# Kernel tuning notes

Measured on AMD Instinct MI355X. Metric: run time of the kernel, lower is better.

The kernel has to match this reference:

```python
import jax, jax.numpy as jnp
import numpy as np


def _conv(x, w, b=None, stride=1, pad=0, dil=1):
    out = jax.lax.conv_general_dilated(
        x, w, (stride, stride), [(pad, pad), (pad, pad)],
        rhs_dilation=(dil, dil),
        dimension_numbers=('NCHW', 'OIHW', 'NCHW'))
    return out if b is None else out + b[None, :, None, None]


def _sobel_base(out_ch, in_ch, k=3):
    # Exactly mirrors SobelConv2d weight construction (4 directional kernels).
    w = np.zeros((out_ch, in_ch, k, k), np.float32)
    m = k // 2
    for idx in range(out_ch):
        if idx % 4 == 0:
            w[idx, :, 0, :] = -1; w[idx, :, 0, m] = -2
            w[idx, :, -1, :] = 1; w[idx, :, -1, m] = 2
        elif idx % 4 == 1:
            w[idx, :, :, 0] = -1; w[idx, :, m, 0] = -2
            w[idx, :, :, -1] = 1; w[idx, :, m, -1] = 2
        elif idx % 4 == 2:
            w[idx, :, 0, 0] = -2
            for i in range(m + 1):
                w[idx, :, m - i, i] = -1
                w[idx, :, k - 1 - i, m + i] = 1
            w[idx, :, -1, -1] = 2
        else:
            w[idx, :, -1, 0] = -2
            for i in range(m + 1):
                w[idx, :, m + i, i] = -1
                w[idx, :, i, m + i] = 1
            w[idx, :, 0, -1] = 2
    return w


def setup_inputs() -> dict:
    key = jax.random.key(0)
    ks = iter(jax.random.split(key, 40))
    def p(shape, s=0.05):
        return jax.random.normal(next(ks), shape, dtype=jnp.float32) * s
    C = 32  # out_ch == sobel_ch
    f32 = jnp.float32
    return dict(
        x=jax.random.normal(next(ks), (8, 1, 256, 256), dtype=f32),
        sobel_base=jnp.asarray(_sobel_base(C, 1)),
        sobel_factor=jnp.ones((C, 1, 1, 1), f32),
        sobel_bias=jnp.zeros((C,), f32),
        f4_w=p((C, C + 1, 3, 3)), f4_b=jnp.zeros((C,), f32),
        ec1_w=p((C, C, 3, 3)), ec1_b=jnp.zeros((C,), f32),
        ec2_w=p((C, C, 3, 3)), ec2_b=jnp.zeros((C,), f32),
        ec3_w=p((C, C, 3, 3)), ec3_b=jnp.zeros((C,), f32),
        gate_w=p((3, 3 * C, 1, 1)), gate_b=jnp.zeros((3,), f32),
        ca1_w=p((C // 16, C, 1, 1)),  # ChannelAttention fc1 (ratio=16), no bias
        ca2_w=p((C, C // 16, 1, 1)),  # fc2, no bias
        sa_w=p((1, 2, 7, 7)),         # SpatialAttention conv, no bias
        p1_w=p((C, C, 1, 1)), p1_b=jnp.zeros((C,), f32),
        f1_w=p((C, C, 3, 3)), f1_b=jnp.zeros((C,), f32),
        p2_w=p((C, 2 * C, 1, 1)), p2_b=jnp.zeros((C,), f32),
        f2_w=p((C, C, 3, 3)), f2_b=jnp.zeros((C,), f32),
        p3_w=p((C, 2 * C, 1, 1)), p3_b=jnp.zeros((C,), f32),
        f3_w=p((C, C, 3, 3)), f3_b=jnp.zeros((C,), f32),
    )


def reference(x, sobel_base, sobel_factor, sobel_bias, f4_w, f4_b,
              ec1_w, ec1_b, ec2_w, ec2_b, ec3_w, ec3_b, gate_w, gate_b,
              ca1_w, ca2_w, sa_w,
              p1_w, p1_b, f1_w, f1_b, p2_w, p2_b, f2_w, f2_b,
              p3_w, p3_b, f3_w, f3_b):
    lrelu = lambda t: jax.nn.leaky_relu(t, 0.01)
    relu = jax.nn.relu
    # Sobel edge extraction (fixed directional kernels scaled by learned factor)
    out0 = _conv(x, sobel_base * sobel_factor, sobel_bias, pad=1)     # [B,32,H,W]
    out1 = jnp.concatenate([x, out0], axis=1)                          # [B,33,H,W]
    out1 = lrelu(_conv(out1, f4_w, f4_b, pad=1))                       # [B,32,H,W]
    # AdaptiveEdgeConnector: multi-dilation convs + softmax gating
    ex = relu(_conv(out1, ec1_w, ec1_b, pad=1))
    ey = relu(_conv(out1, ec2_w, ec2_b, pad=2, dil=2))
    ez = relu(_conv(out1, ec3_w, ec3_b, pad=3, dil=3))
    gates = jax.nn.softmax(_conv(jnp.concatenate([ex, ey, ez], axis=1), gate_w, gate_b), axis=1)
    enh = gates[:, 0:1] * ex + gates[:, 1:2] * ey + gates[:, 2:3] * ez
    # CBAM: channel attention
    avg = jnp.mean(enh, axis=(2, 3), keepdims=True)
    mx = jnp.max(enh, axis=(2, 3), keepdims=True)
    ca = jax.nn.sigmoid(_conv(relu(_conv(avg, ca1_w)), ca2_w)
                        + _conv(relu(_conv(mx, ca1_w)), ca2_w))
    f = ca * enh
    # CBAM: spatial attention
    sa_in = jnp.concatenate([jnp.mean(f, axis=1, keepdims=True),
                             jnp.max(f, axis=1, keepdims=True)], axis=1)
    sa = jax.nn.sigmoid(_conv(sa_in, sa_w, pad=3))
    edge = sa * f
    # Residual merge + cascaded dense conv stages
    out0 = lrelu(out1 + edge)
    t = lrelu(_conv(out0, p1_w, p1_b))
    t = lrelu(_conv(t, f1_w, f1_b, pad=1))
    o1 = jnp.concatenate([out0, t], axis=1)                            # [B,64,H,W]
    t = lrelu(_conv(o1, p2_w, p2_b))
    t = lrelu(_conv(t, f2_w, f2_b, pad=1))
    o2 = jnp.concatenate([out0, t], axis=1)
    t = lrelu(_conv(o2, p3_w, p3_b))
    t = lrelu(_conv(t, f3_w, f3_b, pad=1))
    return jnp.concatenate([out0, t], axis=1)                          # [B,64,H,W]
```

## Files before the change

kernel.cpp:

```cpp
#include <hip/hip_runtime.h>
#include <math.h>

typedef unsigned short u16;
typedef short short8 __attribute__((ext_vector_type(8)));
typedef float f32x4 __attribute__((ext_vector_type(4)));
typedef unsigned short ushort4v __attribute__((ext_vector_type(4)));

#define Hh 256
#define Ww 256
#define Bb 8
#define PW 262
#define PAD 3
#define HPW (Hh * PW)

__device__ __forceinline__ float bf2f(u16 v) {
    unsigned u = ((unsigned)v) << 16;
    union { unsigned u; float f; } c; c.u = u; return c.f;
}
__device__ __forceinline__ u16 f2bf(float f) {
    union { float f; unsigned u; } c; c.f = f;
    unsigned lsb = (c.u >> 16) & 1u;
    c.u += 0x7fffu + lsb;
    return (u16)(c.u >> 16);
}
__device__ __forceinline__ float sigm(float v) { return 1.f / (1.f + expf(-v)); }

template<int ACT, bool F32OUT>
__global__ __launch_bounds__(256) void convs_k(
    const u16* __restrict__ in, const u16* __restrict__ apack,
    const float* __restrict__ bias, void* __restrict__ outp)
{
    __shared__ u16 rows[3][4352];
    const int tid = threadIdx.x, lane = tid & 63, wv = tid >> 6;
    const int b = blockIdx.x & 7;
    const int rest = blockIdx.x >> 3;
    const int h = rest >> 1, half = rest & 1;
    const int pl = wv * 32 + (lane & 15);
    const int icg = lane >> 4;

    for (int idx = tid; idx < 3 * 536; idx += 256) {
        int rr = idx / 536, q = idx % 536;
        int r = h - 1 + rr;
        short8 v = (short8){0, 0, 0, 0, 0, 0, 0, 0};
        if ((unsigned)r < 256u)
            v = *(const short8*)(in + ((size_t)b * HPW + (size_t)r * PW + PAD + half * 128 - 3) * 32
                                 + (size_t)q * 8);
        *(short8*)(&rows[rr][q * 8]) = v;
    }
    __syncthreads();

    f32x4 acc[2][2];
    #pragma unroll
    for (int mf = 0; mf < 2; ++mf)
        #pragma unroll
        for (int nf = 0; nf < 2; ++nf)
            acc[mf][nf] = (f32x4){0.f, 0.f, 0.f, 0.f};

    #pragma unroll
    for (int tap = 0; tap < 9; ++tap) {
        const int kh = tap / 3 - 1, kw = tap % 3 - 1;
        const int ri = 1 + kh;
        short8 a0 = *(const short8*)(apack + ((size_t)(tap * 2 + 0) * 64 + lane) * 8);
        short8 a1 = *(const short8*)(apack + ((size_t)(tap * 2 + 1) * 64 + lane) * 8);
        #pragma unroll
        for (int nf = 0; nf < 2; ++nf) {
            short8 bf = *(const short8*)(&rows[ri][(pl + nf * 16 + kw + 3) * 32 + icg * 8]);
            acc[0][nf] = __builtin_amdgcn_mfma_f32_16x16x32_bf16(a0, bf, acc[0][nf], 0, 0, 0);
            acc[1][nf] = __builtin_amdgcn_mfma_f32_16x16x32_bf16(a1, bf, acc[1][nf], 0, 0, 0);
        }
    }
    const int nl = half * 128 + pl;
    f32x4 bi[2];
    bi[0] = *(const f32x4*)(bias + icg * 4);
    bi[1] = *(const f32x4*)(bias + 16 + icg * 4);
    if (F32OUT) {
        float* dp = (float*)outp + ((size_t)b * 64 + 32) * 65536 + (size_t)h * 256;
        #pragma unroll
        for (int mf = 0; mf < 2; ++mf) {
            const int cob = mf * 16 + icg * 4;
            #pragma unroll
            for (int nf = 0; nf < 2; ++nf) {
                const int w = nl + nf * 16;
                #pragma unroll
                for (int i = 0; i < 4; ++i) {
                    float v = acc[mf][nf][i] + bi[mf][i];
                    if (ACT == 1) v = fmaxf(v, 0.f);
                    if (ACT == 2) v = (v > 0.f) ? v : 0.01f * v;
                    dp[(size_t)(cob + i) * 65536 + w] = v;
                }
            }
        }
    } else {
        const size_t orow = ((size_t)b * HPW + (size_t)h * PW + PAD) * 32;
        u16* out = (u16*)outp;
        #pragma unroll
        for (int mf = 0; mf < 2; ++mf) {
            const int cob = mf * 16 + icg * 4;
            #pragma unroll
            for (int nf = 0; nf < 2; ++nf) {
                ushort4v o;
                #pragma unroll
                for (int i = 0; i < 4; ++i) {
                    float v = acc[mf][nf][i] + bi[mf][i];
                    if (ACT == 1) v = fmaxf(v, 0.f);
                    if (ACT == 2) v = (v > 0.f) ? v : 0.01f * v;
                    o[i] = f2bf(v);
                }
                *(ushort4v*)(out + orow + (size_t)(nl + nf * 16) * 32 + cob) = o;
            }
        }
    }
}

__global__ __launch_bounds__(256) void ecfuse_k(
    const u16* __restrict__ in, const u16* __restrict__ apack,
    const float* __restrict__ b1, const float* __restrict__ b2,
    const float* __restrict__ b3, const float* __restrict__ gw_,
    const float* __restrict__ gb_, u16* __restrict__ enh)
{
    __shared__ u16 rows[3][4352];
    __shared__ float gw[288];
    __shared__ float gb[3];
    __shared__ float bs[96];
    int tid = threadIdx.x;
    for (int i = tid; i < 288; i += 256) gw[i] = gw_[i];
    if (tid < 3) gb[tid] = gb_[tid];
    if (tid < 32) bs[tid] = b1[tid];
    else if (tid < 64) bs[tid] = b2[tid - 32];
    else if (tid < 96) bs[tid] = b3[tid - 64];

    const int lane = tid & 63, wv = tid >> 6;
    const int b = blockIdx.x & 7;
    const int rest = blockIdx.x >> 3;
    const int h = rest >> 1, half = rest & 1;
    const int pl = wv * 32 + (lane & 15);
    const int icg = lane >> 4;

    f32x4 acc[3][2][2];
    #pragma unroll
    for (int cv = 0; cv < 3; ++cv)
        #pragma unroll
        for (int mf = 0; mf < 2; ++mf)
            #pragma unroll
            for (int nf = 0; nf < 2; ++nf)
                acc[cv][mf][nf] = (f32x4){0.f, 0.f, 0.f, 0.f};

    #pragma unroll
    for (int cv = 0; cv < 3; ++cv) {
        const int dil = cv + 1;
        __syncthreads();
        for (int idx = tid; idx < 3 * 536; idx += 256) {
            int rr = idx / 536, q = idx % 536;
            int r = h + (rr - 1) * dil;
            short8 v = (short8){0, 0, 0, 0, 0, 0, 0, 0};
            if ((unsigned)r < 256u)
                v = *(const short8*)(in + ((size_t)b * HPW + (size_t)r * PW + PAD + half * 128 - 3) * 32
                                     + (size_t)q * 8);
            *(short8*)(&rows[rr][q * 8]) = v;
        }
        __syncthreads();
        #pragma unroll
        for (int tap = 0; tap < 9; ++tap) {
            const int kh = tap / 3 - 1, kw = tap % 3 - 1;
            const int ri = 1 + kh;
            const int s = cv * 9 + tap;
            short8 a0 = *(const short8*)(apack + ((size_t)(s * 2 + 0) * 64 + lane) * 8);
            short8 a1 = *(const short8*)(apack + ((size_t)(s * 2 + 1) * 64 + lane) * 8);
            #pragma unroll
            for (int nf = 0; nf < 2; ++nf) {
                short8 bf = *(const short8*)(&rows[ri][(pl + nf * 16 + kw * dil + 3) * 32 + icg * 8]);
                acc[cv][0][nf] = __builtin_amdgcn_mfma_f32_16x16x32_bf16(a0, bf, acc[cv][0][nf], 0, 0, 0);
                acc[cv][1][nf] = __builtin_amdgcn_mfma_f32_16x16x32_bf16(a1, bf, acc[cv][1][nf], 0, 0, 0);
            }
        }
    }
    const int nl = half * 128 + pl;
    const size_t orow = ((size_t)b * HPW + (size_t)h * PW + PAD) * 32;
    #pragma unroll
    for (int nf = 0; nf < 2; ++nf) {
        float e[3][2][4];
        float g0 = 0.f, g1 = 0.f, g2 = 0.f;
        #pragma unroll
        for (int cv = 0; cv < 3; ++cv)
            #pragma unroll
            for (int mf = 0; mf < 2; ++mf) {
                const int cob = mf * 16 + icg * 4;
                #pragma unroll
                for (int i = 0; i < 4; ++i) {
                    float v = fmaxf(acc[cv][mf][nf][i] + bs[cv * 32 + cob + i], 0.f);
                    e[cv][mf][i] = v;
                    const int c = cv * 32 + cob + i;
                    g0 = fmaf(gw[c], v, g0);
                    g1 = fmaf(gw[96 + c], v, g1);
                    g2 = fmaf(gw[192 + c], v, g2);
                }
            }
        g0 += __shfl_xor(g0, 16); g0 += __shfl_xor(g0, 32);
        g1 += __shfl_xor(g1, 16); g1 += __shfl_xor(g1, 32);
        g2 += __shfl_xor(g2, 16); g2 += __shfl_xor(g2, 32);
        g0 += gb[0]; g1 += gb[1]; g2 += gb[2];
        float m = fmaxf(g0, fmaxf(g1, g2));
        float e0 = expf(g0 - m), e1 = expf(g1 - m), e2 = expf(g2 - m);
        float inv = 1.f / (e0 + e1 + e2);
        e0 *= inv; e1 *= inv; e2 *= inv;
        #pragma unroll
        for (int mf = 0; mf < 2; ++mf) {
            const int cob = mf * 16 + icg * 4;
            ushort4v o;
            #pragma unroll
            for (int i = 0; i < 4; ++i)
                o[i] = f2bf(e0 * e[0][mf][i] + e1 * e[1][mf][i] + e2 * e[2][mf][i]);
            *(ushort4v*)(enh + orow + (size_t)(nl + nf * 16) * 32 + cob) = o;
        }
    }
}

template<int ICB, int ACT, bool TWO>
__global__ __launch_bounds__(256) void convm_k(
    const u16* __restrict__ in0, const u16* __restrict__ in1,
    const u16* __restrict__ apack, const float* __restrict__ bias,
    u16* __restrict__ out)
{
    constexpr int CS = TWO ? 32 : ICB * 32;
    const int tid = threadIdx.x, lane = tid & 63, wv = tid >> 6;
    const int b = blockIdx.x & 7, h = blockIdx.x >> 3;
    const int nl = (wv << 6) + (lane & 15);
    const int icg = lane >> 4;

    f32x4 acc[2][4];
    #pragma unroll
    for (int mf = 0; mf < 2; ++mf)
        #pragma unroll
        for (int nf = 0; nf < 4; ++nf)
            acc[mf][nf] = (f32x4){0.f, 0.f, 0.f, 0.f};

    #pragma unroll
    for (int s = 0; s < ICB; ++s) {
        short8 a0 = *(const short8*)(apack + ((size_t)(s * 2 + 0) * 64 + lane) * 8);
        short8 a1 = *(const short8*)(apack + ((size_t)(s * 2 + 1) * 64 + lane) * 8);
        const u16* src = TWO ? (s ? in1 : in0) : in0;
        const int icoff = TWO ? 0 : s * 32;
        size_t base = ((size_t)b * HPW + (size_t)h * PW + PAD + nl) * CS + icoff + icg * 8;
        #pragma unroll
        for (int nf = 0; nf < 4; ++nf) {
            short8 bf = *(const short8*)(src + base + (size_t)nf * 16 * CS);
            acc[0][nf] = __builtin_amdgcn_mfma_f32_16x16x32_bf16(a0, bf, acc[0][nf], 0, 0, 0);
            acc[1][nf] = __builtin_amdgcn_mfma_f32_16x16x32_bf16(a1, bf, acc[1][nf], 0, 0, 0);
        }
    }
    const size_t orow = ((size_t)b * HPW + (size_t)h * PW + PAD) * 32;
    #pragma unroll
    for (int mf = 0; mf < 2; ++mf) {
        const int cob = mf * 16 + icg * 4;
        f32x4 bi = *(const f32x4*)(bias + cob);
        #pragma unroll
        for (int nf = 0; nf < 4; ++nf) {
            ushort4v o;
            #pragma unroll
            for (int i = 0; i < 4; ++i) {
                float v = acc[mf][nf][i] + bi[i];
                if (ACT == 1) v = fmaxf(v, 0.f);
                if (ACT == 2) v = (v > 0.f) ? v : 0.01f * v;
                o[i] = f2bf(v);
            }
            *(ushort4v*)(out + orow + (size_t)(nl + nf * 16) * 32 + cob) = o;
        }
    }
}

__global__ void prepack_k(
    const float* __restrict__ f4w, const float* __restrict__ e1w,
    const float* __restrict__ e2w, const float* __restrict__ e3w,
    const float* __restrict__ f1w, const float* __restrict__ f2w,
    const float* __restrict__ f3w, const float* __restrict__ p1w,
    const float* __restrict__ p2w, const float* __restrict__ p3w,
    u16* __restrict__ apack)
{
    int gid = blockIdx.x * 256 + threadIdx.x;
    if (gid >= 77 * 1024) return;
    const int offs[11] = {0, 18, 27, 36, 45, 54, 63, 72, 73, 75, 77};
    int step = gid >> 10, r = gid & 1023;
    int layer = 0;
    while (step >= offs[layer + 1]) layer++;
    int s = step - offs[layer];
    int mf = r >> 9, l = (r >> 3) & 63, j = r & 7;
    int co = mf * 16 + (l & 15);
    int ICB = (layer == 0 || layer == 8 || layer == 9) ? 2 : 1;
    int tap = s / ICB, icb = s % ICB;
    int icl = icb * 32 + (l >> 4) * 8 + j;
    float v = 0.f;
    if (layer == 0)      { if (icl < 33) v = f4w[(co * 33 + icl) * 9 + tap]; }
    else if (layer == 1) v = e1w[(co * 32 + icl) * 9 + tap];
    else if (layer == 2) v = e2w[(co * 32 + icl) * 9 + tap];
    else if (layer == 3) v = e3w[(co * 32 + icl) * 9 + tap];
    else if (layer == 4) v = f1w[(co * 32 + icl) * 9 + tap];
    else if (layer == 5) v = f2w[(co * 32 + icl) * 9 + tap];
    else if (layer == 6) v = f3w[(co * 32 + icl) * 9 + tap];
    else if (layer == 7) v = p1w[co * 32 + icl];
    else if (layer == 8) v = p2w[co * 64 + icl];
    else                 v = p3w[co * 64 + icl];
    apack[gid] = f2bf(v);
}

__global__ void bzero_k(u16* __restrict__ buf, int total)
{
    int idx = blockIdx.x * 256 + threadIdx.x;
    if (idx >= total) return;
    int c = idx & 31, r = idx >> 5;
    int col6 = r % 6, h = (r / 6) & 255, b = r / (6 * 256);
    int col = (col6 < 3) ? col6 : (256 + PAD + col6 - 3);
    buf[((size_t)b * HPW + (size_t)h * PW + col) * 32 + c] = 0;
}

__global__ __launch_bounds__(256) void prep5_k(
    const float* __restrict__ f4w, const float* __restrict__ f4b,
    const float* __restrict__ sbase, const float* __restrict__ sfac,
    const float* __restrict__ sbias,
    float* __restrict__ w5, float* __restrict__ be)
{
    __shared__ float sF[32 * 33 * 9];
    __shared__ float sS[288];
    __shared__ float sBias[32];
    int t = threadIdx.x;
    for (int i = t; i < 32 * 33 * 9; i += 256) sF[i] = f4w[i];
    for (int i = t; i < 288; i += 256) sS[i] = sbase[i] * sfac[i / 9];
    if (t < 32) sBias[t] = sbias[t];
    __syncthreads();

    for (int idx = t; idx < 800; idx += 256) {
        int co = idx / 25, tap = idx % 25, kh = tap / 5, kw = tap % 5;
        float s = 0.f;
        if (kh >= 1 && kh <= 3 && kw >= 1 && kw <= 3)
            s = sF[(co * 33 + 0) * 9 + (kh - 1) * 3 + (kw - 1)];
        for (int sc = 0; sc < 32; ++sc) {
            #pragma unroll
            for (int a = 0; a < 3; ++a)
                #pragma unroll
                for (int bq = 0; bq < 3; ++bq) {
                    int p = kh - a, q = kw - bq;
                    if (p >= 0 && p < 3 && q >= 0 && q < 3)
                        s = fmaf(sF[(co * 33 + 1 + sc) * 9 + a * 3 + bq],
                                 sS[sc * 9 + p * 3 + q], s);
                }
        }
        w5[idx] = s;
    }
    for (int co = t; co < 32; co += 256) {
        float s = f4b[co];
        for (int sc = 0; sc < 32; ++sc) {
            float wsum = 0.f;
            #pragma unroll
            for (int k = 0; k < 9; ++k) wsum += sF[(co * 33 + 1 + sc) * 9 + k];
            s = fmaf(sBias[sc], wsum, s);
        }
        be[co] = s;
    }
}

__global__ __launch_bounds__(256) void conv5_k(
    const float* __restrict__ x, const float* __restrict__ w5,
    const float* __restrict__ be, u16* __restrict__ out1)
{
    __shared__ float sw[800];
    __shared__ float sb[32];
    int tid = threadIdx.x;
    for (int i = tid; i < 800; i += 256) sw[i] = w5[i];
    if (tid < 32) sb[tid] = be[tid];
    __syncthreads();
    int b = blockIdx.x & 7, h = blockIdx.x >> 3, w = tid;
    const float* xp = x + (size_t)b * 65536;
    float xv[25];
    #pragma unroll
    for (int i = 0; i < 5; ++i) {
        int r = h + i - 2;
        #pragma unroll
        for (int j = 0; j < 5; ++j) {
            int c = w + j - 2;
            xv[i * 5 + j] = ((unsigned)r < 256u && (unsigned)c < 256u)
                            ? xp[r * 256 + c] : 0.f;
        }
    }
    u16* dst = out1 + ((size_t)b * HPW + (size_t)h * PW + PAD + w) * 32;
    #pragma unroll
    for (int cb = 0; cb < 4; ++cb) {
        short8 o;
        #pragma unroll
        for (int j = 0; j < 8; ++j) {
            int co = cb * 8 + j;
            float s = sb[co];
            #pragma unroll
            for (int t2 = 0; t2 < 25; ++t2) s = fmaf(sw[co * 25 + t2], xv[t2], s);
            s = (s > 0.f) ? s : 0.01f * s;
            o[j] = (short)f2bf(s);
        }
        *(short8*)(dst + cb * 8) = o;
    }
}

__global__ __launch_bounds__(256) void ringfix_k(
    const float* __restrict__ x, const float* __restrict__ f4w,
    const float* __restrict__ f4b, const float* __restrict__ sbase,
    const float* __restrict__ sfac, const float* __restrict__ sbias,
    u16* __restrict__ out1)
{
    __shared__ float sW[288];
    __shared__ float sB[32];
    __shared__ float sF[32 * 33 * 9];
    __shared__ float sO[66][2][32];
    int tid = threadIdx.x;
    for (int i = tid; i < 288; i += 256) sW[i] = sbase[i] * sfac[i / 9];
    if (tid < 32) sB[tid] = sbias[tid];
    for (int i = tid; i < 32 * 33 * 9; i += 256) sF[i] = f4w[i];
    __syncthreads();

    int blk = blockIdx.x;
    int b = blk & 7, rest = blk >> 3;
    int e = rest >> 2, seg = rest & 3;
    const float* xp = x + (size_t)b * 65536;

    for (int i = tid; i < 66 * 2 * 32; i += 256) {
        int sc = i & 31, rr2 = i >> 5;
        int d = rr2 & 1, ul = rr2 >> 1;
        int ug = seg * 64 - 1 + ul;
        float v = 0.f;
        if ((unsigned)ug < 256u) {
            int h, w;
            if (e == 0)      { h = d;        w = ug; }
            else if (e == 1) { h = 255 - d;  w = ug; }
            else if (e == 2) { h = ug;       w = d; }
            else             { h = ug;       w = 255 - d; }
            float s = sB[sc];
            for (int p = 0; p < 3; ++p)
                for (int q = 0; q < 3; ++q) {
                    int rr = h + p - 1, cc = w + q - 1;
                    if ((unsigned)rr < 256u && (unsigned)cc < 256u)
                        s = fmaf(sW[sc * 9 + p * 3 + q], xp[rr * 256 + cc], s);
                }
            v = s;
        }
        sO[ul][d][sc] = v;
    }
    __syncthreads();

    int pi = tid & 63, cog = tid >> 6;
    int up = seg * 64 + pi;
    int h, w;
    if (e == 0)      { h = 0;   w = up; }
    else if (e == 1) { h = 255; w = up; }
    else if (e == 2) { h = up;  w = 0; }
    else             { h = up;  w = 255; }
    short8 ov;
    for (int cj = 0; cj < 8; ++cj) {
        int co = cog * 8 + cj;
        float acc = f4b[co];
        for (int a = 0; a < 3; ++a)
            for (int bb = 0; bb < 3; ++bb) {
                int hh = h + a - 1, ww = w + bb - 1;
                if ((unsigned)hh < 256u && (unsigned)ww < 256u)
                    acc = fmaf(sF[(co * 33) * 9 + a * 3 + bb], xp[hh * 256 + ww], acc);
                int d, ug;
                if (e == 0)      { d = hh;        ug = ww; }
                else if (e == 1) { d = 255 - hh;  ug = ww; }
                else if (e == 2) { d = ww;        ug = hh; }
                else             { d = 255 - ww;  ug = hh; }
                if (d >= 0 && d < 2 && (unsigned)ug < 256u) {
                    int ul = ug - (seg * 64 - 1);
                    for (int sc = 0; sc < 32; ++sc)
                        acc = fmaf(sF[(co * 33 + 1 + sc) * 9 + a * 3 + bb], sO[ul][d][sc], acc);
                }
            }
        acc = (acc > 0.f) ? acc : 0.01f * acc;
        ov[cj] = (short)f2bf(acc);
    }
    u16* dst = out1 + ((size_t)b * HPW + (size_t)h * PW + PAD + w) * 32 + cog * 8;
    *(short8*)dst = ov;
}

__global__ __launch_bounds__(256) void ca_part_k(
    const u16* __restrict__ enh, float* __restrict__ part)
{
    int blk = blockIdx.x, b = blk & 7, sl = blk >> 3;
    int tid = threadIdx.x, lane = tid & 63, wv = tid >> 6;
    float s[32], m[32];
    #pragma unroll
    for (int c = 0; c < 32; ++c) { s[c] = 0.f; m[c] = -1e30f; }
    for (int k = 0; k < 8; ++k) {
        int px = sl * 2048 + k * 256 + tid;
        int h = px >> 8, w = px & 255;
        size_t off = ((size_t)b * HPW + (size_t)h * PW + PAD + w) * 32;
        #pragma unroll
        for (int cb = 0; cb < 4; ++cb) {
            short8 v = *(const short8*)(enh + off + cb * 8);
            #pragma unroll
            for (int j = 0; j < 8; ++j) {
                float f = bf2f((u16)v[j]);
                s[cb * 8 + j] += f;
                m[cb * 8 + j] = fmaxf(m[cb * 8 + j], f);
            }
        }
    }
    #pragma unroll
    for (int c = 0; c < 32; ++c)
        #pragma unroll
        for (int o = 32; o; o >>= 1) {
            s[c] += __shfl_down(s[c], o);
            m[c] = fmaxf(m[c], __shfl_down(m[c], o));
        }
    __shared__ float ls[4][32], lm[4][32];
    if (lane == 0)
        for (int c = 0; c < 32; ++c) { ls[wv][c] = s[c]; lm[wv][c] = m[c]; }
    __syncthreads();
    if (tid < 32) {
        float ts = 0.f, tm = -1e30f;
        for (int w2 = 0; w2 < 4; ++w2) { ts += ls[w2][tid]; tm = fmaxf(tm, lm[w2][tid]); }
        int bs = b * 32 + sl;
        part[(size_t)(bs * 2 + 0) * 32 + tid] = ts;
        part[(size_t)(bs * 2 + 1) * 32 + tid] = tm;
    }
}

__global__ void ca_final_k(const float* __restrict__ part,
                           const float* __restrict__ w1, const float* __restrict__ w2,
                           float* __restrict__ ca)
{
    int t = threadIdx.x, b = t >> 5, c = t & 31;
    float s = 0.f, m = -1e30f;
    for (int sl = 0; sl < 32; ++sl) {
        int bs = b * 32 + sl;
        s += part[(size_t)(bs * 2 + 0) * 32 + c];
        m = fmaxf(m, part[(size_t)(bs * 2 + 1) * 32 + c]);
    }
    __shared__ float av[8][32], mx[8][32];
    av[b][c] = s * (1.f / 65536.f);
    mx[b][c] = m;
    __syncthreads();
    float sa0 = 0.f, sm0 = 0.f, sa1 = 0.f, sm1 = 0.f;
    for (int k = 0; k < 32; ++k) {
        float wa = w1[k], wb = w1[32 + k];
        sa0 = fmaf(wa, av[b][k], sa0); sm0 = fmaf(wa, mx[b][k], sm0);
        sa1 = fmaf(wb, av[b][k], sa1); sm1 = fmaf(wb, mx[b][k], sm1);
    }
    float h0 = fmaxf(sa0, 0.f) + fmaxf(sm0, 0.f);
    float h1 = fmaxf(sa1, 0.f) + fmaxf(sm1, 0.f);
    ca[t] = sigm(w2[c * 2 + 0] * h0 + w2[c * 2 + 1] * h1);
}

__global__ __launch_bounds__(256) void samap_k(
    const u16* __restrict__ enh, const float* __restrict__ ca,
    float* __restrict__ smap)
{
    __shared__ float sca[256];
    int tid = threadIdx.x;
    sca[tid] = ca[tid];
    __syncthreads();
    int b = blockIdx.x & 7;
    int r = (blockIdx.x >> 3) * 256 + tid;
    if (r >= 262 * 262) return;
    int ph = r / 262, pw = r % 262;
    float mean = 0.f, mxv = 0.f;
    if (ph >= 3 && ph < 259 && pw >= 3 && pw < 259) {
        int h = ph - 3, w = pw - 3;
        size_t off = ((size_t)b * HPW + (size_t)h * PW + PAD + w) * 32;
        float s = 0.f, m = -1e30f;
        #pragma unroll
        for (int cb = 0; cb < 4; ++cb) {
            short8 v = *(const short8*)(enh + off + cb * 8);
            #pragma unroll
            for (int j = 0; j < 8; ++j) {
                float f = bf2f((u16)v[j]) * sca[b * 32 + cb * 8 + j];
                s += f; m = fmaxf(m, f);
            }
        }
        mean = s * (1.f / 32.f); mxv = m;
    }
    smap[((size_t)b * 262 * 262 + (size_t)ph * 262 + pw) * 2 + 0] = mean;
    smap[((size_t)b * 262 * 262 + (size_t)ph * 262 + pw) * 2 + 1] = mxv;
}

__global__ __launch_bounds__(256) void merge_k(
    const float* __restrict__ smap, const float* __restrict__ saw,
    const float* __restrict__ ca, const u16* __restrict__ out1,
    const u16* __restrict__ enh, u16* __restrict__ o0,
    float* __restrict__ dout)
{
    __shared__ float sw[98];
    __shared__ float sca[256];
    int tid = threadIdx.x;
    for (int i = tid; i < 98; i += 256) sw[i] = saw[i];
    sca[tid] = ca[tid];
    __syncthreads();
    int b = blockIdx.x & 7;
    int hw = (blockIdx.x >> 3) * 256 + tid;
    int h = hw >> 8, w = hw & 255;
    const float* sp = smap + (size_t)b * 262 * 262 * 2;
    float acc = 0.f;
    #pragma unroll
    for (int kh = 0; kh < 7; ++kh)
        #pragma unroll
        for (int kw = 0; kw < 7; ++kw) {
            const float* q = sp + ((size_t)(h + kh) * 262 + (w + kw)) * 2;
            acc = fmaf(q[0], sw[kh * 7 + kw], acc);
            acc = fmaf(q[1], sw[49 + kh * 7 + kw], acc);
        }
    float sa = sigm(acc);
    size_t off = ((size_t)b * HPW + (size_t)h * PW + PAD + w) * 32;
    float* dp = dout + (size_t)b * 64 * 65536 + hw;
    #pragma unroll
    for (int cb = 0; cb < 4; ++cb) {
        short8 ve = *(const short8*)(enh + off + cb * 8);
        short8 vo = *(const short8*)(out1 + off + cb * 8);
        short8 o;
        #pragma unroll
        for (int j = 0; j < 8; ++j) {
            float f = sca[b * 32 + cb * 8 + j] * bf2f((u16)ve[j]);
            float v = bf2f((u16)vo[j]) + sa * f;
            v = (v > 0.f) ? v : 0.01f * v;
            o[j] = (short)f2bf(v);
            dp[(size_t)(cb * 8 + j) * 65536] = v;
        }
        *(short8*)(o0 + off + cb * 8) = o;
    }
}

extern "C" void kernel_launch(void* const* d_in, const int* in_sizes, int n_in,
                              void* d_out, int out_size, void* d_ws, size_t ws_size,
                              hipStream_t stream)
{
    (void)in_sizes; (void)n_in; (void)out_size; (void)ws_size;
    const float* x        = (const float*)d_in[0];
    const float* sob_base = (const float*)d_in[1];
    const float* sob_fac  = (const float*)d_in[2];
    const float* sob_bias = (const float*)d_in[3];
    const float* f4_w = (const float*)d_in[4];   const float* f4_b = (const float*)d_in[5];
    const float* ec1_w = (const float*)d_in[6];  const float* ec1_b = (const float*)d_in[7];
    const float* ec2_w = (const float*)d_in[8];  const float* ec2_b = (const float*)d_in[9];
    const float* ec3_w = (const float*)d_in[10]; const float* ec3_b = (const float*)d_in[11];
    const float* gate_w = (const float*)d_in[12]; const float* gate_b = (const float*)d_in[13];
    const float* ca1_w = (const float*)d_in[14]; const float* ca2_w = (const float*)d_in[15];
    const float* sa_w  = (const float*)d_in[16];
    const float* p1_w = (const float*)d_in[17]; const float* p1_b = (const float*)d_in[18];
    const float* f1_w = (const float*)d_in[19]; const float* f1_b = (const float*)d_in[20];
    const float* p2_w = (const float*)d_in[21]; const float* p2_b = (const float*)d_in[22];
    const float* f2_w = (const float*)d_in[23]; const float* f2_b = (const float*)d_in[24];
    const float* p3_w = (const float*)d_in[25]; const float* p3_b = (const float*)d_in[26];
    const float* f3_w = (const float*)d_in[27]; const float* f3_b = (const float*)d_in[28];

    const size_t PB32 = (size_t)Bb * HPW * 32 * 2;
    char* ws = (char*)d_ws;
    u16* Q    = (u16*)(ws);
    u16* O0   = (u16*)(ws + PB32);
    u16* T    = (u16*)(ws + 2 * PB32);
    u16* ENH  = (u16*)(ws + 3 * PB32);
    u16* AP   = (u16*)(ws + 4 * PB32);
    float* W5   = (float*)(ws + 4 * PB32 + 77 * 1024 * 2);
    float* BE   = W5 + 800;
    float* PART = BE + 32;
    float* CA   = PART + 8 * 32 * 2 * 32;

    char* doutc = (char*)d_out;
    float* SMAP = (float*)(doutc + (134217728 - (size_t)Bb * 262 * 262 * 2 * 4));
    float* dout = (float*)d_out;

    dim3 blk(256);

    prepack_k<<<308, blk, 0, stream>>>(f4_w, ec1_w, ec2_w, ec3_w, f1_w, f2_w, f3_w,
                                       p1_w, p2_w, p3_w, AP);
    prep5_k<<<1, blk, 0, stream>>>(f4_w, f4_b, sob_base, sob_fac, sob_bias, W5, BE);
    bzero_k<<<1536, blk, 0, stream>>>(Q, Bb * 256 * 6 * 32);
    bzero_k<<<1536, blk, 0, stream>>>(T, Bb * 256 * 6 * 32);
    conv5_k<<<2048, blk, 0, stream>>>(x, W5, BE, Q);
    ringfix_k<<<128, blk, 0, stream>>>(x, f4_w, f4_b, sob_base, sob_fac, sob_bias, Q);
    ecfuse_k<<<4096, blk, 0, stream>>>(Q, AP + 18 * 1024, ec1_b, ec2_b, ec3_b,
                                       gate_w, gate_b, ENH);
    ca_part_k<<<256, blk, 0, stream>>>(ENH, PART);
    ca_final_k<<<1, blk, 0, stream>>>(PART, ca1_w, ca2_w, CA);
    samap_k<<<2152, blk, 0, stream>>>(ENH, CA, SMAP);
    merge_k<<<2048, blk, 0, stream>>>(SMAP, sa_w, CA, Q, ENH, O0, dout);
    convm_k<1, 2, false><<<2048, blk, 0, stream>>>(O0, nullptr, AP + 72 * 1024, p1_b, Q);
    convs_k<2, false><<<4096, blk, 0, stream>>>(Q, AP + 45 * 1024, f1_b, T);
    convm_k<2, 2, true ><<<2048, blk, 0, stream>>>(O0, T, AP + 73 * 1024, p2_b, Q);
    convs_k<2, false><<<4096, blk, 0, stream>>>(Q, AP + 54 * 1024, f2_b, T);
    convm_k<2, 2, true ><<<2048, blk, 0, stream>>>(O0, T, AP + 75 * 1024, p3_b, Q);
    convs_k<2, true ><<<4096, blk, 0, stream>>>(Q, AP + 63 * 1024, f3_b, dout);
}
```

Before: 437.8 us.

## Swizzle LDS row layout, prefetch weight fragments, stage f32 outputs through LDS

Reorganises the shared-memory row buffers in the 3x3 conv kernels into channel-group-major order to reduce bank conflicts on MFMA operand reads, and prefetches the next tap's weight fragments into registers. The fp32 output stores in the final conv and merge kernels are staged through LDS and written as 16-byte vectors. One zero-fill launch for the T buffer is dropped, which relies on its halo columns staying zero otherwise. The extra LDS tile in merge may reduce occupancy.

```diff
diff --git a/kernel.cpp b/kernel.cpp
--- a/kernel.cpp
+++ b/kernel.cpp
@@ -24,6 +24,7 @@
     return (u16)(c.u >> 16);
 }
 __device__ __forceinline__ float sigm(float v) { return 1.f / (1.f + expf(-v)); }
+
 
 template<int ACT, bool F32OUT>
 __global__ __launch_bounds__(256) void convs_k(
@@ -40,12 +41,13 @@
 
     for (int idx = tid; idx < 3 * 536; idx += 256) {
         int rr = idx / 536, q = idx % 536;
+        int p = q >> 2, g = q & 3;
         int r = h - 1 + rr;
         short8 v = (short8){0, 0, 0, 0, 0, 0, 0, 0};
         if ((unsigned)r < 256u)
             v = *(const short8*)(in + ((size_t)b * HPW + (size_t)r * PW + PAD + half * 128 - 3) * 32
-                                 + (size_t)q * 8);
-        *(short8*)(&rows[rr][q * 8]) = v;
+                                 + (size_t)p * 32 + g * 8);
+        *(short8*)(&rows[rr][(g * 136 + p) * 8]) = v;
     }
     __syncthreads();
 
@@ -56,40 +58,54 @@
         for (int nf = 0; nf < 2; ++nf)
             acc[mf][nf] = (f32x4){0.f, 0.f, 0.f, 0.f};
 
+    short8 a0c = *(const short8*)(apack + (size_t)(0 * 2 + 0) * 512 + lane * 8);
+    short8 a1c = *(const short8*)(apack + (size_t)(0 * 2 + 1) * 512 + lane * 8);
     #pragma unroll
     for (int tap = 0; tap < 9; ++tap) {
         const int kh = tap / 3 - 1, kw = tap % 3 - 1;
         const int ri = 1 + kh;
-        short8 a0 = *(const short8*)(apack + ((size_t)(tap * 2 + 0) * 64 + lane) * 8);
-        short8 a1 = *(const short8*)(apack + ((size_t)(tap * 2 + 1) * 64 + lane) * 8);
+        short8 a0n, a1n;
+        if (tap < 8) {
+            a0n = *(const short8*)(apack + (size_t)((tap + 1) * 2 + 0) * 512 + lane * 8);
+            a1n = *(const short8*)(apack + (size_t)((tap + 1) * 2 + 1) * 512 + lane * 8);
+        }
         #pragma unroll
         for (int nf = 0; nf < 2; ++nf) {
-            short8 bf = *(const short8*)(&rows[ri][(pl + nf * 16 + kw + 3) * 32 + icg * 8]);
-            acc[0][nf] = __builtin_amdgcn_mfma_f32_16x16x32_bf16(a0, bf, acc[0][nf], 0, 0, 0);
-            acc[1][nf] = __builtin_amdgcn_mfma_f32_16x16x32_bf16(a1, bf, acc[1][nf], 0, 0, 0);
-        }
+            short8 bf = *(const short8*)(&rows[ri][(icg * 136 + pl + nf * 16 + kw + 3) * 8]);
+            acc[0][nf] = __builtin_amdgcn_mfma_f32_16x16x32_bf16(a0c, bf, acc[0][nf], 0, 0, 0);
+            acc[1][nf] = __builtin_amdgcn_mfma_f32_16x16x32_bf16(a1c, bf, acc[1][nf], 0, 0, 0);
+        }
+        a0c = a0n; a1c = a1n;
     }
     const int nl = half * 128 + pl;
     f32x4 bi[2];
     bi[0] = *(const f32x4*)(bias + icg * 4);
     bi[1] = *(const f32x4*)(bias + 16 + icg * 4);
     if (F32OUT) {
-        float* dp = (float*)outp + ((size_t)b * 64 + 32) * 65536 + (size_t)h * 256;
+        float* ldsf = (float*)&rows[0][0];
+        __syncthreads();
         #pragma unroll
         for (int mf = 0; mf < 2; ++mf) {
             const int cob = mf * 16 + icg * 4;
             #pragma unroll
             for (int nf = 0; nf < 2; ++nf) {
-                const int w = nl + nf * 16;
+                const int pxl = pl + nf * 16;
                 #pragma unroll
                 for (int i = 0; i < 4; ++i) {
                     float v = acc[mf][nf][i] + bi[mf][i];
                     if (ACT == 1) v = fmaxf(v, 0.f);
                     if (ACT == 2) v = (v > 0.f) ? v : 0.01f * v;
-                    dp[(size_t)(cob + i) * 65536 + w] = v;
+                    ldsf[(cob + i) * 128 + pxl] = v;
                 }
             }
         }
+        __syncthreads();
+        const int ch = tid >> 3, pxb = (tid & 7) * 16;
+        float* dp = (float*)outp + ((size_t)b * 64 + 32 + ch) * 65536
+                    + (size_t)h * 256 + half * 128 + pxb;
+        #pragma unroll
+        for (int j = 0; j < 4; ++j)
+            *(f32x4*)(dp + j * 4) = *(f32x4*)(&ldsf[ch * 128 + pxb + j * 4]);
     } else {
         const size_t orow = ((size_t)b * HPW + (size_t)h * PW + PAD) * 32;
         u16* out = (u16*)outp;
@@ -151,27 +167,34 @@
         __syncthreads();
         for (int idx = tid; idx < 3 * 536; idx += 256) {
             int rr = idx / 536, q = idx % 536;
+            int p = q >> 2, g = q & 3;
             int r = h + (rr - 1) * dil;
             short8 v = (short8){0, 0, 0, 0, 0, 0, 0, 0};
             if ((unsigned)r < 256u)
                 v = *(const short8*)(in + ((size_t)b * HPW + (size_t)r * PW + PAD + half * 128 - 3) * 32
-                                     + (size_t)q * 8);
-            *(short8*)(&rows[rr][q * 8]) = v;
+                                     + (size_t)p * 32 + g * 8);
+            *(short8*)(&rows[rr][(g * 136 + p) * 8]) = v;
         }
         __syncthreads();
+        const u16* ap = apack + (size_t)(cv * 9 * 2) * 512;
+        short8 a0c = *(const short8*)(ap + (size_t)0 * 512 + lane * 8);
+        short8 a1c = *(const short8*)(ap + (size_t)1 * 512 + lane * 8);
         #pragma unroll
         for (int tap = 0; tap < 9; ++tap) {
             const int kh = tap / 3 - 1, kw = tap % 3 - 1;
             const int ri = 1 + kh;
-            const int s = cv * 9 + tap;
-            short8 a0 = *(const short8*)(apack + ((size_t)(s * 2 + 0) * 64 + lane) * 8);
-            short8 a1 = *(const short8*)(apack + ((size_t)(s * 2 + 1) * 64 + lane) * 8);
+            short8 a0n, a1n;
+            if (tap < 8) {
+                a0n = *(const short8*)(ap + (size_t)((tap + 1) * 2 + 0) * 512 + lane * 8);
+                a1n = *(const short8*)(ap + (size_t)((tap + 1) * 2 + 1) * 512 + lane * 8);
+            }
             #pragma unroll
             for (int nf = 0; nf < 2; ++nf) {
-                short8 bf = *(const short8*)(&rows[ri][(pl + nf * 16 + kw * dil + 3) * 32 + icg * 8]);
-                acc[cv][0][nf] = __builtin_amdgcn_mfma_f32_16x16x32_bf16(a0, bf, acc[cv][0][nf], 0, 0, 0);
-                acc[cv][1][nf] = __builtin_amdgcn_mfma_f32_16x16x32_bf16(a1, bf, acc[cv][1][nf], 0, 0, 0);
-            }
+                short8 bf = *(const short8*)(&rows[ri][(icg * 136 + pl + nf * 16 + kw * dil + 3) * 8]);
+                acc[cv][0][nf] = __builtin_amdgcn_mfma_f32_16x16x32_bf16(a0c, bf, acc[cv][0][nf], 0, 0, 0);
+                acc[cv][1][nf] = __builtin_amdgcn_mfma_f32_16x16x32_bf16(a1c, bf, acc[cv][1][nf], 0, 0, 0);
+            }
+            a0c = a0n; a1c = a1n;
         }
     }
     const int nl = half * 128 + pl;
@@ -585,13 +608,14 @@
 {
     __shared__ float sw[98];
     __shared__ float sca[256];
+    __shared__ float tile[32 * 256];
     int tid = threadIdx.x;
     for (int i = tid; i < 98; i += 256) sw[i] = saw[i];
     sca[tid] = ca[tid];
     __syncthreads();
     int b = blockIdx.x & 7;
-    int hw = (blockIdx.x >> 3) * 256 + tid;
-    int h = hw >> 8, w = hw & 255;
+    int h = blockIdx.x >> 3;
+    int w = tid;
     const float* sp = smap + (size_t)b * 262 * 262 * 2;
     float acc = 0.f;
     #pragma unroll
@@ -604,7 +628,6 @@
         }
     float sa = sigm(acc);
     size_t off = ((size_t)b * HPW + (size_t)h * PW + PAD + w) * 32;
-    float* dp = dout + (size_t)b * 64 * 65536 + hw;
     #pragma unroll
     for (int cb = 0; cb < 4; ++cb) {
         short8 ve = *(const short8*)(enh + off + cb * 8);
@@ -616,10 +639,16 @@
             float v = bf2f((u16)vo[j]) + sa * f;
             v = (v > 0.f) ? v : 0.01f * v;
             o[j] = (short)f2bf(v);
-            dp[(size_t)(cb * 8 + j) * 65536] = v;
+            tile[(cb * 8 + j) * 256 + w] = v;
         }
         *(short8*)(o0 + off + cb * 8) = o;
     }
+    __syncthreads();
+    const int ch = tid >> 3, pxb = (tid & 7) * 32;
+    float* dp = dout + ((size_t)b * 64 + ch) * 65536 + (size_t)h * 256 + pxb;
+    #pragma unroll
+    for (int j = 0; j < 8; ++j)
+        *(f32x4*)(dp + j * 4) = *(f32x4*)(&tile[ch * 256 + pxb + j * 4]);
 }
 
 extern "C" void kernel_launch(void* const* d_in, const int* in_sizes, int n_in,
@@ -667,7 +696,6 @@
                                        p1_w, p2_w, p3_w, AP);
     prep5_k<<<1, blk, 0, stream>>>(f4_w, f4_b, sob_base, sob_fac, sob_bias, W5, BE);
     bzero_k<<<1536, blk, 0, stream>>>(Q, Bb * 256 * 6 * 32);
-    bzero_k<<<1536, blk, 0, stream>>>(T, Bb * 256 * 6 * 32);
     conv5_k<<<2048, blk, 0, stream>>>(x, W5, BE, Q);
     ringfix_k<<<128, blk, 0, stream>>>(x, f4_w, f4_b, sob_base, sob_fac, sob_bias, Q);
     ecfuse_k<<<4096, blk, 0, stream>>>(Q, AP + 18 * 1024, ec1_b, ec2_b, ec3_b,
```

Measured after the change: 461.4 us. +5.4%, slower.
